# Performance work log

Hardware: AMD Instinct MI355X
Metric: run time of the kernel (lower is better)

## Reference

```python
import jax, jax.numpy as jnp
import numpy as np

B, Cin, H, W = 4, 64, 160, 160
Cout, K, STRIDE, PAD = 64, 3, 1, 1
KK = K * K


def setup_inputs() -> dict:
    key = jax.random.key(0)
    ks = jax.random.split(key, 4)
    x = jax.random.normal(ks[0], (B, Cin, H, W), jnp.float32)
    # offset/mask conv params (zero-init in source; small random so offsets are non-trivial)
    offset_w = jax.random.normal(ks[1], (3 * KK, Cin, K, K), jnp.float32) * 0.01
    offset_b = jax.random.normal(ks[2], (3 * KK,), jnp.float32) * 0.01
    fan_in = Cin * K * K
    weight = jax.random.normal(ks[3], (Cout, Cin, K, K), jnp.float32) / np.sqrt(fan_in)
    bias = jnp.zeros((Cout,), jnp.float32)
    return dict(x=x, offset_w=offset_w, offset_b=offset_b, weight=weight, bias=bias)


def _conv2d(x, w, b):
    y = jax.lax.conv_general_dilated(
        x, w, window_strides=(STRIDE, STRIDE),
        padding=[(PAD, PAD), (PAD, PAD)],
        dimension_numbers=('NCHW', 'OIHW', 'NCHW'))
    return y + b[None, :, None, None]


def _deform_conv2d(x, offset, mask, weight, bias):
    # x: [B,C,H,W]; offset: [B,2*KK,Ho,Wo] as (dy,dx) pairs; mask: [B,KK,Ho,Wo]
    Bs, C, Hh, Ww = x.shape
    Ho, Wo = offset.shape[2], offset.shape[3]
    off = offset.reshape(Bs, KK, 2, Ho, Wo)
    dy, dx = off[:, :, 0], off[:, :, 1]            # [B,KK,Ho,Wo]
    ki, kj = jnp.meshgrid(jnp.arange(K), jnp.arange(K), indexing='ij')
    ki = ki.reshape(KK).astype(jnp.float32)
    kj = kj.reshape(KK).astype(jnp.float32)
    hb = (jnp.arange(Ho) * STRIDE - PAD).astype(jnp.float32)
    wb = (jnp.arange(Wo) * STRIDE - PAD).astype(jnp.float32)
    py = dy + ki[None, :, None, None] + hb[None, None, :, None]  # sample y coords
    px = dx + kj[None, :, None, None] + wb[None, None, None, :]  # sample x coords
    y0 = jnp.floor(py); x0 = jnp.floor(px)
    wy1 = py - y0; wy0 = 1.0 - wy1
    wx1 = px - x0; wx0 = 1.0 - wx1
    x_hwc = jnp.transpose(x, (0, 2, 3, 1))          # [B,H,W,C]

    def corner(yc, xc):
        valid = (yc >= 0) & (yc < Hh) & (xc >= 0) & (xc < Ww)
        yi = jnp.clip(yc, 0, Hh - 1).astype(jnp.int32)
        xi = jnp.clip(xc, 0, Ww - 1).astype(jnp.int32)
        g = jax.vmap(lambda img, yy, xx: img[yy, xx])(x_hwc, yi, xi)  # [B,KK,Ho,Wo,C]
        return g * valid[..., None].astype(x.dtype)

    val = (corner(y0, x0) * (wy0 * wx0)[..., None]
           + corner(y0, x0 + 1.0) * (wy0 * wx1)[..., None]
           + corner(y0 + 1.0, x0) * (wy1 * wx0)[..., None]
           + corner(y0 + 1.0, x0 + 1.0) * (wy1 * wx1)[..., None])
    val = val * mask[..., None]                      # modulated (DCNv2)
    w2 = weight.reshape(weight.shape[0], C, KK)      # [O,C,KK]
    out = jnp.einsum('bkhwc,ock->bohw', val, w2)
    return out + bias[None, :, None, None]


def reference(x, offset_w, offset_b, weight, bias):
    out = _conv2d(x, offset_w, offset_b)             # [B,3*KK,Ho,Wo]
    o1, o2, m = jnp.split(out, 3, axis=1)
    offset = jnp.concatenate([o1, o2], axis=1)       # [B,2*KK,Ho,Wo]
    mask = jax.nn.sigmoid(m)
    return _deform_conv2d(x, offset, mask, weight, bias)
```

## Files before the change

kernel.cpp:

```cpp
#include <hip/hip_runtime.h>
#include <hip/hip_bf16.h>
#include <math.h>

#define B_ 4
#define CIN 64
#define H_ 160
#define W_ 160
#define COUT 64
#define KK_ 9
#define HW_ (H_ * W_)
#define KTOT 576
#define CP32 200
#define XPITCH 72
#define SL32 33
#define NT32 3200
#define TPX32 400

typedef __attribute__((ext_vector_type(8))) short bf16x8;
typedef __attribute__((ext_vector_type(4))) float f32x4;

__device__ inline unsigned short f2bf(float f) {
    unsigned int u = __float_as_uint(f);
    u = (u + 0x7FFF + ((u >> 16) & 1)) >> 16;
    return (unsigned short)u;
}

__device__ inline unsigned short bfc(float f) {
    __hip_bfloat16 h = __float2bfloat16(f);
    union { __hip_bfloat16 h; unsigned short u; } cv;
    cv.h = h;
    return cv.u;
}

__global__ __launch_bounds__(256) void prep_all_k(const float* __restrict__ x,
                                                  const float* __restrict__ wgt,
                                                  const float* __restrict__ ow,
                                                  float* __restrict__ xt,
                                                  unsigned short* __restrict__ wB,
                                                  unsigned short* __restrict__ wB2) {
    __shared__ float tile[64][65];
    int bid = blockIdx.x;
    int t = threadIdx.x;

    if (bid < 1600) {
        int pbk = bid % 400, b = bid / 400;
        int p0 = pbk * 64;
        const float* xp = x + (size_t)b * CIN * HW_ + p0;

        int pg = (t & 15) * 4, cr = t >> 4;
#pragma unroll
        for (int i = 0; i < 4; i++) {
            int c = i * 16 + cr;
            float4 v = *(const float4*)(xp + (size_t)c * HW_ + pg);
            tile[c][pg]     = v.x;
            tile[c][pg + 1] = v.y;
            tile[c][pg + 2] = v.z;
            tile[c][pg + 3] = v.w;
        }
        __syncthreads();

        int c4 = (t & 15) * 4, pr = t >> 4;
        float* op = xt + ((size_t)b * HW_ + p0) * 64 + c4;
#pragma unroll
        for (int i = 0; i < 4; i++) {
            int p = i * 16 + pr;
            float4 v;
            v.x = tile[c4][p];
            v.y = tile[c4 + 1][p];
            v.z = tile[c4 + 2][p];
            v.w = tile[c4 + 3][p];
            *(float4*)(op + (size_t)p * 64) = v;
        }
    } else if (bid < 1744) {
        int i = (bid - 1600) * 256 + t;
        int o = i / KTOT, r = i % KTOT;
        int tap = r >> 6, c = r & 63;
        wB[i] = f2bf(wgt[(o * CIN + c) * KK_ + tap]);
    } else {
        int i = (bid - 1744) * 256 + t;
        int n = i / KTOT, r = i % KTOT;
        int tap = r >> 6, c = r & 63;
        wB2[i] = (n < 27) ? f2bf(ow[(n * CIN + c) * KK_ + tap]) : (unsigned short)0;
    }
}

__global__ __launch_bounds__(256, 5) void fused_dcn_k(const float* __restrict__ xt,
                                                      const unsigned short* __restrict__ wB2,
                                                      const float* __restrict__ ob,
                                                      const unsigned short* __restrict__ wB,
                                                      const float* __restrict__ bias,
                                                      float* __restrict__ out) {
    __shared__ __align__(16) char ubuf[14688];
    __shared__ __align__(16) char pbuf[288 * 32];
    __shared__ float slog[27 * SL32];
    unsigned short* sX  = (unsigned short*)ubuf;
    unsigned short* sAc = (unsigned short*)ubuf;
    float4* spar_w = (float4*)pbuf;
    int4*   spar_o = (int4*)(pbuf + 288 * 16);

    int t = threadIdx.x;
    int lane = t & 63, wv = t >> 6;
    int bid = blockIdx.x;
    int tile = (bid & 7) * TPX32 + (bid >> 3);
    int gp0 = tile * 32;
    int wo0 = gp0 % W_;
    int tmp = gp0 / W_;
    int ho = tmp % H_;
    int b  = tmp / H_;

    const float* xb = xt + (size_t)b * HW_ * 64 + lane;

    for (int i = 0; i < 26; i++) {
        int r = i * 4 + wv;
        if (r < 102) {
            int yy = ho - 1 + r / 34;
            int xx = wo0 - 1 + r % 34;
            float v = 0.f;
            if (yy >= 0 && yy < H_ && xx >= 0 && xx < W_)
                v = xb[(size_t)(yy * W_ + xx) * 64];
            sX[r * XPITCH + lane] = bfc(v);
        }
    }
    __syncthreads();

    {
        int m = lane & 15, q = lane >> 4;
        int h  = wv >> 1;
        int ocl = (wv & 1) * 16 + m;
        float bv = (ocl < 27) ? ob[ocl] : 0.f;
        f32x4 acc  = {bv, bv, bv, bv};
        f32x4 acc2 = {0.f, 0.f, 0.f, 0.f};
        const unsigned short* brow = wB2 + ocl * KTOT + q * 8;
#pragma unroll
        for (int tap = 0; tap < 9; tap++) {
            int row = (tap / 3) * 34 + (tap % 3) + h * 16 + m;
            const unsigned short* sxr = sX + row * XPITCH + q * 8;
            bf16x8 af0 = *(const bf16x8*)(sxr);
            bf16x8 af1 = *(const bf16x8*)(sxr + 32);
            bf16x8 b0  = *(const bf16x8*)(brow + (2 * tap) * 32);
            bf16x8 b1  = *(const bf16x8*)(brow + (2 * tap + 1) * 32);
            acc  = __builtin_amdgcn_mfma_f32_16x16x32_bf16(af0, b0, acc,  0, 0, 0);
            acc2 = __builtin_amdgcn_mfma_f32_16x16x32_bf16(af1, b1, acc2, 0, 0, 0);
        }
#pragma unroll
        for (int r = 0; r < 4; r++) acc[r] += acc2[r];
        if (ocl < 27) {
            float* sl = slog + ocl * SL32 + h * 16 + q * 4;
            if (ocl < 18) {
#pragma unroll
                for (int r = 0; r < 4; r++) sl[r] = acc[r];
            } else {
#pragma unroll
                for (int r = 0; r < 4; r++) sl[r] = 1.f / (1.f + expf(-acc[r]));
            }
        }
    }
    __syncthreads();

    for (int l = lane; l < 72; l += 64) {
        int task = l * 4 + wv;
        int p = task & 31, k = task >> 5;
        float dyv = slog[(2 * k) * SL32 + p];
        float dxv = slog[(2 * k + 1) * SL32 + p];
        float mv  = slog[(18 + k) * SL32 + p];
        float py = dyv + (float)(k / 3) + (float)(ho - 1);
        float px = dxv + (float)(k % 3) + (float)(wo0 + p - 1);
        float y0f = floorf(py), x0f = floorf(px);
        float wy1 = py - y0f, wx1 = px - x0f;
        float wy0 = 1.f - wy1, wx0 = 1.f - wx1;
        int y0 = (int)y0f, x0 = (int)x0f;
        bool yv0 = (y0 >= 0) && (y0 < H_);
        bool yv1 = (y0 + 1 >= 0) && (y0 + 1 < H_);
        bool xv0 = (x0 >= 0) && (x0 < W_);
        bool xv1 = (x0 + 1 >= 0) && (x0 + 1 < W_);
        float4 w4;
        w4.x = (yv0 && xv0) ? wy0 * wx0 * mv : 0.f;
        w4.y = (yv0 && xv1) ? wy0 * wx1 * mv : 0.f;
        w4.z = (yv1 && xv0) ? wy1 * wx0 * mv : 0.f;
        w4.w = (yv1 && xv1) ? wy1 * wx1 * mv : 0.f;
        spar_w[task] = w4;
        int yc0 = min(max(y0, 0), H_ - 1), yc1 = min(max(y0 + 1, 0), H_ - 1);
        int xc0 = min(max(x0, 0), W_ - 1), xc1 = min(max(x0 + 1, 0), W_ - 1);
        int4 o4;
        o4.x = (yc0 * W_ + xc0) * 256;
        o4.y = (yc0 * W_ + xc1) * 256;
        o4.z = (yc1 * W_ + xc0) * 256;
        o4.w = (yc1 * W_ + xc1) * 256;
        spar_o[task] = o4;
    }
    __asm__ volatile("s_waitcnt lgkmcnt(0)" ::: "memory");

    int m = lane & 15, q = lane >> 4;
    int o0 = wv * 16 + m;
    float b0v = bias[o0];
    f32x4 acc00 = {b0v, b0v, b0v, b0v};
    f32x4 acc01 = {0.f, 0.f, 0.f, 0.f};
    f32x4 acc10 = {b0v, b0v, b0v, b0v};
    f32x4 acc11 = {0.f, 0.f, 0.f, 0.f};
    const unsigned short* br0 = wB + o0 * KTOT + q * 8;
    const unsigned short* arow0 = sAc + m * CP32 + q * 8;
    const unsigned short* arow1 = sAc + (16 + m) * CP32 + q * 8;

    unsigned lane4 = (unsigned)lane << 2;
    const char* xu = (const char*)xt + (size_t)b * ((size_t)HW_ * 64 * 4);

#pragma unroll
    for (int c = 0; c < 3; c++) {
#pragma unroll
        for (int g = 0; g < 2; g++) {
            float v00[12], v01[12], v10[12], v11[12];
#pragma unroll
            for (int j = 0; j < 12; j++) {
                int task = 96 * c + (g * 12 + j) * 4 + wv;
                int4 o4 = spar_o[task];
                v00[j] = *(const float*)(xu + ((unsigned)o4.x + lane4));
                v01[j] = *(const float*)(xu + ((unsigned)o4.y + lane4));
                v10[j] = *(const float*)(xu + ((unsigned)o4.z + lane4));
                v11[j] = *(const float*)(xu + ((unsigned)o4.w + lane4));
            }
#pragma unroll
            for (int j = 0; j < 12; j++) {
                int task = 96 * c + (g * 12 + j) * 4 + wv;
                float4 w4 = spar_w[task];
                int p = task & 31, kc = (task >> 5) - 3 * c;
                float v = v00[j] * w4.x + v01[j] * w4.y
                        + v10[j] * w4.z + v11[j] * w4.w;
                sAc[p * CP32 + kc * 64 + lane] = bfc(v);
            }
        }
        __syncthreads();

#pragma unroll
        for (int tl = 0; tl < 3; tl++) {
            bf16x8 b0  = *(const bf16x8*)(br0 + ((c * 3 + tl) * 2) * 32);
            bf16x8 b1  = *(const bf16x8*)(br0 + ((c * 3 + tl) * 2 + 1) * 32);
            bf16x8 a00 = *(const bf16x8*)(arow0 + (2 * tl) * 32);
            bf16x8 a01 = *(const bf16x8*)(arow0 + (2 * tl + 1) * 32);
            bf16x8 a10 = *(const bf16x8*)(arow1 + (2 * tl) * 32);
            bf16x8 a11 = *(const bf16x8*)(arow1 + (2 * tl + 1) * 32);
            acc00 = __builtin_amdgcn_mfma_f32_16x16x32_bf16(a00, b0, acc00, 0, 0, 0);
            acc01 = __builtin_amdgcn_mfma_f32_16x16x32_bf16(a01, b1, acc01, 0, 0, 0);
            acc10 = __builtin_amdgcn_mfma_f32_16x16x32_bf16(a10, b0, acc10, 0, 0, 0);
            acc11 = __builtin_amdgcn_mfma_f32_16x16x32_bf16(a11, b1, acc11, 0, 0, 0);
        }
        if (c < 2) __syncthreads();
    }

#pragma unroll
    for (int r = 0; r < 4; r++) { acc00[r] += acc01[r]; acc10[r] += acc11[r]; }

    size_t a0 = ((size_t)(b * COUT + o0)) * HW_ + (size_t)ho * W_ + wo0 + q * 4;
    float4 r0; r0.x = acc00[0]; r0.y = acc00[1]; r0.z = acc00[2]; r0.w = acc00[3];
    *(float4*)(out + a0) = r0;
    float4 r1; r1.x = acc10[0]; r1.y = acc10[1]; r1.z = acc10[2]; r1.w = acc10[3];
    *(float4*)(out + a0 + 16) = r1;
}

extern "C" void kernel_launch(void* const* d_in, const int* in_sizes, int n_in,
                              void* d_out, int out_size, void* d_ws, size_t ws_size,
                              hipStream_t stream) {
    const float* x    = (const float*)d_in[0];
    const float* ow   = (const float*)d_in[1];
    const float* ob   = (const float*)d_in[2];
    const float* wgt  = (const float*)d_in[3];
    const float* bias = (const float*)d_in[4];
    float* out = (float*)d_out;

    float* ws  = (float*)d_ws;
    float* xt  = ws;
    unsigned short* wB  = (unsigned short*)(xt + (size_t)B_ * HW_ * CIN);
    unsigned short* wB2 = wB + (size_t)COUT * KTOT;

    prep_all_k<<<1816, 256, 0, stream>>>(x, wgt, ow, xt, wB, wB2);
    fused_dcn_k<<<NT32, 256, 0, stream>>>(xt, wB2, ob, wB, bias, out);
}
```

Before: 183.1 us.

## Use 2x16 output tiles to shrink halo, compress gather offsets, raise occupancy

Changes each block's 32-pixel tile from a 1x32 row strip to a 2x16 patch, so the input halo for the offset conv falls from 102 to 72 rows and less shared memory is needed. Bilinear corner offsets are packed into a base plus packed dy/dx deltas (int2 instead of int4), which cuts the parameter LDS footprint. Launch bounds go from 5 to 7 blocks per CU to exploit the smaller LDS use. Risks include register pressure from the higher occupancy target and less coalesced 16-wide stores and gathers.

```diff
diff --git a/kernel.cpp b/kernel.cpp
--- a/kernel.cpp
+++ b/kernel.cpp
@@ -84,42 +84,41 @@
     }
 }
 
-__global__ __launch_bounds__(256, 5) void fused_dcn_k(const float* __restrict__ xt,
+__global__ __launch_bounds__(256, 7) void fused_dcn_k(const float* __restrict__ xt,
                                                       const unsigned short* __restrict__ wB2,
                                                       const float* __restrict__ ob,
                                                       const unsigned short* __restrict__ wB,
                                                       const float* __restrict__ bias,
                                                       float* __restrict__ out) {
-    __shared__ __align__(16) char ubuf[14688];
-    __shared__ __align__(16) char pbuf[288 * 32];
+    __shared__ __align__(16) char ubuf[12800];
+    __shared__ __align__(16) char pbuf[288 * 24];
     __shared__ float slog[27 * SL32];
     unsigned short* sX  = (unsigned short*)ubuf;
     unsigned short* sAc = (unsigned short*)ubuf;
     float4* spar_w = (float4*)pbuf;
-    int4*   spar_o = (int4*)(pbuf + 288 * 16);
+    int2*   spar_o = (int2*)(pbuf + 288 * 16);
 
     int t = threadIdx.x;
     int lane = t & 63, wv = t >> 6;
     int bid = blockIdx.x;
-    int tile = (bid & 7) * TPX32 + (bid >> 3);
-    int gp0 = tile * 32;
-    int wo0 = gp0 % W_;
-    int tmp = gp0 / W_;
-    int ho = tmp % H_;
-    int b  = tmp / H_;
+    int t2 = (bid & 7) * TPX32 + (bid >> 3);
+    int b  = t2 / 800;
+    int ti = t2 % 800;
+    int ho  = (ti / 10) * 2;
+    int wo0 = (ti % 10) * 16;
 
     const float* xb = xt + (size_t)b * HW_ * 64 + lane;
 
-    for (int i = 0; i < 26; i++) {
+#pragma unroll
+    for (int i = 0; i < 18; i++) {
         int r = i * 4 + wv;
-        if (r < 102) {
-            int yy = ho - 1 + r / 34;
-            int xx = wo0 - 1 + r % 34;
-            float v = 0.f;
-            if (yy >= 0 && yy < H_ && xx >= 0 && xx < W_)
-                v = xb[(size_t)(yy * W_ + xx) * 64];
-            sX[r * XPITCH + lane] = bfc(v);
-        }
+        int ry = r / 18, rx = r % 18;
+        int yy = ho - 1 + ry;
+        int xx = wo0 - 1 + rx;
+        float v = 0.f;
+        if (yy >= 0 && yy < H_ && xx >= 0 && xx < W_)
+            v = xb[(size_t)(yy * W_ + xx) * 64];
+        sX[r * XPITCH + lane] = bfc(v);
     }
     __syncthreads();
 
@@ -133,7 +132,7 @@
         const unsigned short* brow = wB2 + ocl * KTOT + q * 8;
 #pragma unroll
         for (int tap = 0; tap < 9; tap++) {
-            int row = (tap / 3) * 34 + (tap % 3) + h * 16 + m;
+            int row = (h + tap / 3) * 18 + m + (tap % 3);
             const unsigned short* sxr = sX + row * XPITCH + q * 8;
             bf16x8 af0 = *(const bf16x8*)(sxr);
             bf16x8 af1 = *(const bf16x8*)(sxr + 32);
@@ -160,11 +159,12 @@
     for (int l = lane; l < 72; l += 64) {
         int task = l * 4 + wv;
         int p = task & 31, k = task >> 5;
+        int h = p >> 4, col = p & 15;
         float dyv = slog[(2 * k) * SL32 + p];
         float dxv = slog[(2 * k + 1) * SL32 + p];
         float mv  = slog[(18 + k) * SL32 + p];
-        float py = dyv + (float)(k / 3) + (float)(ho - 1);
-        float px = dxv + (float)(k % 3) + (float)(wo0 + p - 1);
+        float py = dyv + (float)(k / 3) + (float)(ho + h - 1);
+        float px = dxv + (float)(k % 3) + (float)(wo0 + col - 1);
         float y0f = floorf(py), x0f = floorf(px);
         float wy1 = py - y0f, wx1 = px - x0f;
         float wy0 = 1.f - wy1, wx0 = 1.f - wx1;
@@ -181,12 +181,11 @@
         spar_w[task] = w4;
         int yc0 = min(max(y0, 0), H_ - 1), yc1 = min(max(y0 + 1, 0), H_ - 1);
         int xc0 = min(max(x0, 0), W_ - 1), xc1 = min(max(x0 + 1, 0), W_ - 1);
-        int4 o4;
-        o4.x = (yc0 * W_ + xc0) * 256;
-        o4.y = (yc0 * W_ + xc1) * 256;
-        o4.z = (yc1 * W_ + xc0) * 256;
-        o4.w = (yc1 * W_ + xc1) * 256;
-        spar_o[task] = o4;
+        int base  = (yc0 * W_ + xc0) * 256;
+        int dyoff = (yc1 - yc0) * (W_ * 256);
+        int dxoff = (xc1 - xc0) * 256;
+        int2 o2; o2.x = base; o2.y = (dyoff << 16) | dxoff;
+        spar_o[task] = o2;
     }
     __asm__ volatile("s_waitcnt lgkmcnt(0)" ::: "memory");
 
@@ -212,11 +211,14 @@
 #pragma unroll
             for (int j = 0; j < 12; j++) {
                 int task = 96 * c + (g * 12 + j) * 4 + wv;
-                int4 o4 = spar_o[task];
-                v00[j] = *(const float*)(xu + ((unsigned)o4.x + lane4));
-                v01[j] = *(const float*)(xu + ((unsigned)o4.y + lane4));
-                v10[j] = *(const float*)(xu + ((unsigned)o4.z + lane4));
-                v11[j] = *(const float*)(xu + ((unsigned)o4.w + lane4));
+                int2 o2 = spar_o[task];
+                unsigned base = (unsigned)o2.x + lane4;
+                unsigned dyo  = (unsigned)o2.y >> 16;
+                unsigned dxo  = (unsigned)o2.y & 0xffffu;
+                v00[j] = *(const float*)(xu + base);
+                v01[j] = *(const float*)(xu + base + dxo);
+                v10[j] = *(const float*)(xu + base + dyo);
+                v11[j] = *(const float*)(xu + base + dyo + dxo);
             }
 #pragma unroll
             for (int j = 0; j < 12; j++) {
@@ -253,7 +255,7 @@
     float4 r0; r0.x = acc00[0]; r0.y = acc00[1]; r0.z = acc00[2]; r0.w = acc00[3];
     *(float4*)(out + a0) = r0;
     float4 r1; r1.x = acc10[0]; r1.y = acc10[1]; r1.z = acc10[2]; r1.w = acc10[3];
-    *(float4*)(out + a0 + 16) = r1;
+    *(float4*)(out + a0 + W_) = r1;
 }
 
 extern "C" void kernel_launch(void* const* d_in, const int* in_sizes, int n_in,
```

Result: slower. 190.3 us (+3.9%).
